# Kernel optimization log

Hardware: AMD Instinct MI355X
Metric: run time of the kernel (lower is better)

Reference implementation:

```python
import jax, jax.numpy as jnp
import numpy as np

N_FR, N_FV, N_REL, N_VAL, N_KN = 512, 512, 256, 256, 512
TOPK_FR, TOPK_FV, TOPK_REL, TOPK_VAL = 8, 8, 4, 6
EPS = 1e-8


def setup_inputs() -> dict:
    key = jax.random.key(0)
    k1, k2, k3, k4 = jax.random.split(key, 4)
    B, S, D, DS = 8, 2048, 2048, 64
    N = N_FR + N_FV + N_REL + N_VAL + N_KN  # 2304
    return {
        "x": jax.random.normal(k1, (B, S, D), dtype=jnp.float32),
        "importance": jax.random.uniform(k2, (B, S), dtype=jnp.float32),
        "W": jax.random.normal(k3, (DS, D), dtype=jnp.float32) * (1.0 / np.sqrt(D)),
        "b": jnp.zeros((DS,), dtype=jnp.float32),
        "neuron_emb": jax.random.normal(k4, (N, DS), dtype=jnp.float32) * 0.02,
    }


def _topk_sparsify(w, k):
    # w: [B, n] -> keep top-k values, zero the rest, renormalize to sum 1
    vals, idx = jax.lax.top_k(w, k)
    B = w.shape[0]
    sparse = jnp.zeros_like(w).at[jnp.arange(B)[:, None], idx].set(vals)
    return sparse / (sparse.sum(axis=-1, keepdims=True) + EPS)


def reference(x, importance, W, b, neuron_emb):
    # Projection (nn.Linear): [B,S,d_space]; dropout is identity in eval mode
    h = jnp.einsum('bsd,kd->bsk', x, W) + b
    # Normalized neuron embeddings (F.normalize along dim=-1)
    emb = neuron_emb / jnp.linalg.norm(neuron_emb, axis=-1, keepdims=True)
    # All routing logits in one shot: [B, S, total_neurons]
    all_logits = jnp.einsum('bsk,nk->bsn', h, emb)

    fr_end = N_FR
    fv_end = N_FR + N_FV
    rel_end = fv_end + N_REL
    val_end = rel_end + N_VAL

    fr_pref = jax.nn.softmax(all_logits[..., :fr_end], axis=-1)
    fv_pref = jax.nn.softmax(all_logits[..., fr_end:fv_end], axis=-1)
    rel_pref = jax.nn.softmax(all_logits[..., fv_end:rel_end], axis=-1)  # shared by Q and K
    val_pref = jax.nn.softmax(all_logits[..., rel_end:val_end], axis=-1)

    def dense(pref):
        return jnp.einsum('bs,bsn->bn', importance, pref)

    fr_w = _topk_sparsify(dense(fr_pref), TOPK_FR)
    fv_w = _topk_sparsify(dense(fv_pref), TOPK_FV)
    rel_d = dense(rel_pref)
    rq_w = _topk_sparsify(rel_d, TOPK_REL)
    rk_w = rq_w  # relational_Q and relational_K slices are identical
    val_w = _topk_sparsify(dense(val_pref), TOPK_VAL)

    # Concatenate the five per-batch routing weight vectors: [B, 512+512+256+256+256]
    return jnp.concatenate([fr_w, fv_w, rq_w, rk_w, val_w], axis=-1)
```

## Files before the change

### kernel.cpp

```cpp
#include <hip/hip_runtime.h>
#include <hip/hip_bf16.h>

#define B_    8
#define S_    2048
#define D_    2048
#define DS_   64
#define NUSED 1536
#define TOK   16384

typedef __attribute__((ext_vector_type(8))) short bf16x8;
typedef __attribute__((ext_vector_type(4))) float f32x4;

static constexpr int WS_ETF  = 0;
static constexpr int WS_HT   = 98304;
static constexpr int WS_PART = 2195456;
static constexpr int WS_PART2= 3768320;
static constexpr int WS_WF   = 3866624;

typedef __attribute__((address_space(1))) const void g_void;
typedef __attribute__((address_space(3))) void l_void;

__device__ inline short bf_hi(float f, float& rhi) {
    __hip_bfloat16 h = __float2bfloat16(f);
    rhi = __bfloat162float(h);
    return __builtin_bit_cast(short, h);
}
__device__ inline short bf_of(float f) {
    __hip_bfloat16 h = __float2bfloat16(f);
    return __builtin_bit_cast(short, h);
}
__device__ inline int sliceOfTile(int tile) {
    return tile < 32 ? 0 : tile < 64 ? 1 : tile < 80 ? 2 : 3;
}

__launch_bounds__(256)
__global__ void k_pre(const float* __restrict__ emb, const float* __restrict__ W,
                      short* __restrict__ etfrag, short* __restrict__ wfrag) {
    __shared__ float red[2][16][8];
    __shared__ float rn[2][16];
    const int tid = threadIdx.x;
    if (blockIdx.x < 48) {
        const int tl = tid >> 7, tid2 = tid & 127;
        const int kh = tid2 >> 6, lane = tid2 & 63;
        const int tile = blockIdx.x * 2 + tl;
        const int nl = lane & 15;
        const int n = tile * 16 + nl;
        const int kb = kh * 32 + (lane >> 4) * 8;
        const float* ep = emb + n * DS_ + kb;
        float4 a = *reinterpret_cast<const float4*>(ep);
        float4 b = *reinterpret_cast<const float4*>(ep + 4);
        float f[8] = {a.x, a.y, a.z, a.w, b.x, b.y, b.z, b.w};
        float ss = 0.f;
#pragma unroll
        for (int j = 0; j < 8; ++j) ss += f[j] * f[j];
        red[tl][nl][kh * 4 + (lane >> 4)] = ss;
        __syncthreads();
        if (tid2 < 16) {
            float s = 0.f;
#pragma unroll
            for (int j = 0; j < 8; ++j) s += red[tl][tid2][j];
            rn[tl][tid2] = 1.0f / sqrtf(s);
        }
        __syncthreads();
        const float r0 = rn[tl][nl];
        bf16x8 hi, lo;
#pragma unroll
        for (int j = 0; j < 8; ++j) {
            float v = f[j] * r0, r;
            hi[j] = bf_hi(v, r);
            lo[j] = bf_of(v - r);
        }
        short* dst = etfrag + (size_t)((tile * 2 + kh) * 64 + lane) * 16;
        *reinterpret_cast<bf16x8*>(dst)     = hi;
        *reinterpret_cast<bf16x8*>(dst + 8) = lo;
    } else {
        const int kstep = blockIdx.x - 48;
        const int msub = tid >> 6, lane = tid & 63;
        const int m = msub * 16 + (lane & 15);
        const float* wp = W + m * D_ + kstep * 32 + (lane >> 4) * 8;
        float4 a = *reinterpret_cast<const float4*>(wp);
        float4 b = *reinterpret_cast<const float4*>(wp + 4);
        float f[8] = {a.x, a.y, a.z, a.w, b.x, b.y, b.z, b.w};
        bf16x8 hi, lo;
#pragma unroll
        for (int j = 0; j < 8; ++j) {
            float r;
            hi[j] = bf_hi(f[j], r);
            lo[j] = bf_of(f[j] - r);
        }
        short* base = wfrag + (size_t)(kstep * 4 + msub) * 1024;
        *reinterpret_cast<bf16x8*>(base + lane * 8)       = hi;
        *reinterpret_cast<bf16x8*>(base + 512 + lane * 8) = lo;
    }
}

#define MFMA16(A, Bv, C) __builtin_amdgcn_mfma_f32_16x16x32_bf16(A, Bv, C, 0, 0, 0)

__launch_bounds__(256, 2)
__global__ void k_gemm1(const float* __restrict__ x, const short* __restrict__ wfrag,
                        float* __restrict__ htp) {
    __shared__ short wlds[2][4][4096];

    const int tid   = threadIdx.x;
    const int split = blockIdx.x & 1;
    const int tb    = (blockIdx.x >> 1) * 64;
    const int wave  = tid >> 6, lane = tid & 63;
    const int tok   = tb + wave * 16 + (lane & 15);

    const float* xp   = x + (size_t)tok * D_ + split * 1024 + (lane >> 4) * 8;
    const short* wsrc = wfrag + (size_t)(split * 32) * 4096;

    f32x4 acc0 = {0.f, 0.f, 0.f, 0.f};
    f32x4 acc1 = acc0, acc2 = acc0, acc3 = acc0;

#define STAGE4(gg, buf)                                                                      \
    {                                                                                        \
        _Pragma("unroll")                                                                    \
        for (int s = 0; s < 4; ++s) {                                                        \
            const short* s0 = wsrc + (size_t)(4 * (gg) + s) * 4096;                          \
            __builtin_amdgcn_global_load_lds((g_void*)(s0 + tid * 8),                        \
                                             (l_void*)(&wlds[buf][s][tid * 8]), 16, 0, 0);   \
            __builtin_amdgcn_global_load_lds((g_void*)(s0 + 2048 + tid * 8),                 \
                                             (l_void*)(&wlds[buf][s][2048 + tid * 8]), 16, 0, 0); \
        }                                                                                    \
    }

    STAGE4(0, 0);
    float4 xc[4], xn[4];
#pragma unroll
    for (int i = 0; i < 4; ++i)
        xc[i] = *reinterpret_cast<const float4*>(xp + (i >> 1) * 32 + (i & 1) * 4);

    for (int g = 0; g < 8; ++g) {
        __syncthreads();
        const int buf = g & 1;
        if (g < 7) STAGE4(g + 1, buf ^ 1);

#pragma unroll
        for (int half = 0; half < 2; ++half) {
            const int hh = g * 2 + half;
            if (hh < 15) {
                const float* nxp = xp + (size_t)(hh + 1) * 64;
#pragma unroll
                for (int i = 0; i < 4; ++i)
                    xn[i] = *reinterpret_cast<const float4*>(nxp + (i >> 1) * 32 + (i & 1) * 4);
            }
#pragma unroll
            for (int kk2 = 0; kk2 < 2; ++kk2) {
                const int kk = half * 2 + kk2;
                const float4 va = xc[kk2 * 2], vb = xc[kk2 * 2 + 1];
                float xf[8] = {va.x, va.y, va.z, va.w, vb.x, vb.y, vb.z, vb.w};
                bf16x8 bh, bl;
#pragma unroll
                for (int j = 0; j < 8; ++j) {
                    float r;
                    bh[j] = bf_hi(xf[j], r);
                    bl[j] = bf_of(xf[j] - r);
                }
                const short* wl = &wlds[buf][kk][0];
                bf16x8 ah0 = *reinterpret_cast<const bf16x8*>(wl +    0 + lane * 8);
                bf16x8 al0 = *reinterpret_cast<const bf16x8*>(wl +  512 + lane * 8);
                bf16x8 ah1 = *reinterpret_cast<const bf16x8*>(wl + 1024 + lane * 8);
                bf16x8 al1 = *reinterpret_cast<const bf16x8*>(wl + 1536 + lane * 8);
                bf16x8 ah2 = *reinterpret_cast<const bf16x8*>(wl + 2048 + lane * 8);
                bf16x8 al2 = *reinterpret_cast<const bf16x8*>(wl + 2560 + lane * 8);
                bf16x8 ah3 = *reinterpret_cast<const bf16x8*>(wl + 3072 + lane * 8);
                bf16x8 al3 = *reinterpret_cast<const bf16x8*>(wl + 3584 + lane * 8);

                acc0 = MFMA16(ah0, bh, acc0);
                acc1 = MFMA16(ah1, bh, acc1);
                acc2 = MFMA16(ah2, bh, acc2);
                acc3 = MFMA16(ah3, bh, acc3);
                acc0 = MFMA16(al0, bh, acc0);
                acc1 = MFMA16(al1, bh, acc1);
                acc2 = MFMA16(al2, bh, acc2);
                acc3 = MFMA16(al3, bh, acc3);
                acc0 = MFMA16(ah0, bl, acc0);
                acc1 = MFMA16(ah1, bl, acc1);
                acc2 = MFMA16(ah2, bl, acc2);
                acc3 = MFMA16(ah3, bl, acc3);
            }
            if (hh < 15) {
#pragma unroll
                for (int i = 0; i < 4; ++i) xc[i] = xn[i];
            }
        }
    }

    const int row0 = split * 64 + (lane >> 4) * 4;
    const int col  = tb + wave * 16 + (lane & 15);
#pragma unroll
    for (int r = 0; r < 4; ++r) {
        htp[(size_t)(row0 +  0 + r) * TOK + col] = acc0[r];
        htp[(size_t)(row0 + 16 + r) * TOK + col] = acc1[r];
        htp[(size_t)(row0 + 32 + r) * TOK + col] = acc2[r];
        htp[(size_t)(row0 + 48 + r) * TOK + col] = acc3[r];
    }
}

__launch_bounds__(512)
__global__ void k_route2(const float* __restrict__ htp, const float* __restrict__ bias,
                         const short* __restrict__ etfrag, const float* __restrict__ imp,
                         float* __restrict__ part) {
    __shared__ float h_lds[64][32];
    __shared__ float zw[2][8][2][16];
    __shared__ float coef[2][4][16];
    __shared__ float impb[32];

    const int tid = threadIdx.x;
    const int w = tid >> 6, lane = tid & 63;
    const int tt2 = blockIdx.x;
    const int tk = lane & 15, g = lane >> 4;

    {
        const int k = tid >> 3, c8 = tid & 7;
        const float4* hp4 = reinterpret_cast<const float4*>(htp);
        const int col = tt2 * 8 + c8;
        float4 a = hp4[(size_t)k * 4096 + col];
        float4 b = hp4[(size_t)(k + 64) * 4096 + col];
        float bk = bias[k];
        float4 s;
        s.x = a.x + b.x + bk;
        s.y = a.y + b.y + bk;
        s.z = a.z + b.z + bk;
        s.w = a.w + b.w + bk;
        *reinterpret_cast<float4*>(&h_lds[k][c8 * 4]) = s;
    }
    if (tid < 32) impb[tid] = imp[tt2 * 32 + tid];
    __syncthreads();

    bf16x8 bh0A, bl0A, bh1A, bl1A, bh0B, bl0B, bh1B, bl1B;
#pragma unroll
    for (int j = 0; j < 8; ++j) {
        float r, v;
        v = h_lds[g * 8 + j][tk];           bh0A[j] = bf_hi(v, r); bl0A[j] = bf_of(v - r);
        v = h_lds[32 + g * 8 + j][tk];      bh1A[j] = bf_hi(v, r); bl1A[j] = bf_of(v - r);
        v = h_lds[g * 8 + j][16 + tk];      bh0B[j] = bf_hi(v, r); bl0B[j] = bf_of(v - r);
        v = h_lds[32 + g * 8 + j][16 + tk]; bh1B[j] = bf_hi(v, r); bl1B[j] = bf_of(v - r);
    }

    const int t0 = w * 12;
    const int sA = sliceOfTile(t0);
    const int sB = sliceOfTile(t0 + 11);
    float zA0 = 0.f, zA1 = 0.f, zB0 = 0.f, zB1 = 0.f;
    float pA[12][4], pB[12][4];

    const short* ep = etfrag + (size_t)t0 * 2048 + lane * 16;
#pragma unroll
    for (int ti = 0; ti < 12; ++ti) {
        const short* cp = ep + (size_t)ti * 2048;
        bf16x8 ah0 = *reinterpret_cast<const bf16x8*>(cp);
        bf16x8 al0 = *reinterpret_cast<const bf16x8*>(cp + 8);
        bf16x8 ah1 = *reinterpret_cast<const bf16x8*>(cp + 1024);
        bf16x8 al1 = *reinterpret_cast<const bf16x8*>(cp + 1032);
        f32x4 a0 = {0.f, 0.f, 0.f, 0.f};
        f32x4 a1 = a0, b0 = a0, b1 = a0;
        a0 = MFMA16(ah0, bh0A, a0);  b0 = MFMA16(ah0, bh0B, b0);
        a1 = MFMA16(ah1, bh1A, a1);  b1 = MFMA16(ah1, bh1B, b1);
        a0 = MFMA16(al0, bh0A, a0);  b0 = MFMA16(al0, bh0B, b0);
        a1 = MFMA16(al1, bh1A, a1);  b1 = MFMA16(al1, bh1B, b1);
        a0 = MFMA16(ah0, bl0A, a0);  b0 = MFMA16(ah0, bl0B, b0);
        a1 = MFMA16(ah1, bl1A, a1);  b1 = MFMA16(ah1, bl1B, b1);

        const float pa0 = __expf(a0[0] + a1[0]);
        const float pa1 = __expf(a0[1] + a1[1]);
        const float pa2 = __expf(a0[2] + a1[2]);
        const float pa3 = __expf(a0[3] + a1[3]);
        pA[ti][0] = pa0; pA[ti][1] = pa1; pA[ti][2] = pa2; pA[ti][3] = pa3;
        const float zsA = (pa0 + pa1) + (pa2 + pa3);
        const float pb0 = __expf(b0[0] + b1[0]);
        const float pb1 = __expf(b0[1] + b1[1]);
        const float pb2 = __expf(b0[2] + b1[2]);
        const float pb3 = __expf(b0[3] + b1[3]);
        pB[ti][0] = pb0; pB[ti][1] = pb1; pB[ti][2] = pb2; pB[ti][3] = pb3;
        const float zsB = (pb0 + pb1) + (pb2 + pb3);
        if (sliceOfTile(t0 + ti) == sA) { zA0 += zsA; zB0 += zsB; }
        else                            { zA1 += zsA; zB1 += zsB; }
    }

    zA0 += __shfl_xor(zA0, 16); zA0 += __shfl_xor(zA0, 32);
    zA1 += __shfl_xor(zA1, 16); zA1 += __shfl_xor(zA1, 32);
    zB0 += __shfl_xor(zB0, 16); zB0 += __shfl_xor(zB0, 32);
    zB1 += __shfl_xor(zB1, 16); zB1 += __shfl_xor(zB1, 32);
    if (lane < 16) {
        zw[0][w][0][lane] = zA0; zw[0][w][1][lane] = zA1;
        zw[1][w][0][lane] = zB0; zw[1][w][1][lane] = zB1;
    }
    __syncthreads();

    if (tid < 128) {
        const int tl = tid >> 6, s = (tid >> 4) & 3, k2 = tid & 15;
        float z = 0.f;
#pragma unroll
        for (int w2 = 0; w2 < 8; ++w2) {
            const int a = sliceOfTile(w2 * 12);
            const int b = sliceOfTile(w2 * 12 + 11);
            if (a == s) z += zw[tl][w2][0][k2];
            if (b == s && b != a) z += zw[tl][w2][1][k2];
        }
        coef[tl][s][k2] = impb[tl * 16 + k2] / z;
    }
    __syncthreads();

    const float cAA = coef[0][sA][tk], cAB = coef[0][sB][tk];
    const float cBA = coef[1][sA][tk], cBB = coef[1][sB][tk];
    float* poutA = part + (size_t)(tt2 * 2) * NUSED;
    float* poutB = poutA + NUSED;
#pragma unroll
    for (int ti = 0; ti < 12; ++ti) {
        const bool inA = (sliceOfTile(t0 + ti) == sA);
        {
            const float c = inA ? cAA : cAB;
            float v0 = pA[ti][0] * c, v1 = pA[ti][1] * c, v2 = pA[ti][2] * c, v3 = pA[ti][3] * c;
#pragma unroll
            for (int st = 1; st < 16; st <<= 1) {
                v0 += __shfl_xor(v0, st);
                v1 += __shfl_xor(v1, st);
                v2 += __shfl_xor(v2, st);
                v3 += __shfl_xor(v3, st);
            }
            if (tk == 0)
                *reinterpret_cast<float4*>(&poutA[(t0 + ti) * 16 + g * 4]) =
                    make_float4(v0, v1, v2, v3);
        }
        {
            const float c = inA ? cBA : cBB;
            float v0 = pB[ti][0] * c, v1 = pB[ti][1] * c, v2 = pB[ti][2] * c, v3 = pB[ti][3] * c;
#pragma unroll
            for (int st = 1; st < 16; st <<= 1) {
                v0 += __shfl_xor(v0, st);
                v1 += __shfl_xor(v1, st);
                v2 += __shfl_xor(v2, st);
                v3 += __shfl_xor(v3, st);
            }
            if (tk == 0)
                *reinterpret_cast<float4*>(&poutB[(t0 + ti) * 16 + g * 4]) =
                    make_float4(v0, v1, v2, v3);
        }
    }
}

__launch_bounds__(256)
__global__ void kA(const float* __restrict__ part, float* __restrict__ part2) {
    const int tid = threadIdx.x;
    const int b = blockIdx.x >> 3, g = blockIdx.x & 7;
    const int base = (b * 128 + g * 16) * NUSED;
#pragma unroll
    for (int i = 0; i < 6; ++i) {
        int n = tid + 256 * i;
        float s = 0.f;
#pragma unroll
        for (int r = 0; r < 16; ++r) s += part[base + r * NUSED + n];
        part2[(b * 8 + g) * NUSED + n] = s;
    }
}

__launch_bounds__(256)
__global__ void kB(const float* __restrict__ part2, float* __restrict__ out) {
    __shared__ float dens[NUSED];
    __shared__ float s_v[4][8];
    __shared__ int   s_n[4][8];
    const int tid = threadIdx.x;
    const int b = blockIdx.x;

#pragma unroll
    for (int i = 0; i < 6; ++i) {
        int n = tid + 256 * i;
        float s = 0.f;
#pragma unroll
        for (int g = 0; g < 8; ++g) s += part2[(b * 8 + g) * NUSED + n];
        dens[n] = s;
    }
    for (int i = tid; i < 1792; i += 256) out[b * 1792 + i] = 0.f;
    __syncthreads();

    const int w = tid >> 6, lane = tid & 63;
    const int soffs[4] = {0, 512, 1024, 1280};
    const int ssz[4]   = {512, 512, 256, 256};
    const int kks[4]   = {8, 8, 4, 6};
    const int ooffs[4] = {0, 512, 1024, 1536};
    const int Sn = ssz[w], soff = soffs[w], kk = kks[w];
    const int nslots = Sn >> 6;

    float v[8];
#pragma unroll
    for (int i = 0; i < 8; ++i)
        v[i] = (i < nslots) ? dens[soff + lane + 64 * i] : -1e30f;

    unsigned rm = 0;
    float ssum = 0.f;
    for (int it = 0; it < kk; ++it) {
        float bv = -1e30f;
        int bn = 0x7fffffff;
#pragma unroll
        for (int i = 0; i < 8; ++i) {
            bool valid = (i < nslots) && !((rm >> i) & 1u);
            if (valid && v[i] > bv) { bv = v[i]; bn = lane + 64 * i; }
        }
#pragma unroll
        for (int off = 32; off; off >>= 1) {
            float ov = __shfl_xor(bv, off);
            int   on = __shfl_xor(bn, off);
            if (ov > bv || (ov == bv && on < bn)) { bv = ov; bn = on; }
        }
        ssum += bv;
        if ((bn & 63) == lane) rm |= 1u << (bn >> 6);
        if (lane == 0) { s_v[w][it] = bv; s_n[w][it] = bn; }
    }
    const float inv = 1.f / (ssum + 1e-8f);
    if (lane < kk) {
        int n = s_n[w][lane];
        float val = s_v[w][lane] * inv;
        out[b * 1792 + ooffs[w] + n] = val;
        if (w == 2) out[b * 1792 + 1280 + n] = val;
    }
}

extern "C" void kernel_launch(void* const* d_in, const int* in_sizes, int n_in,
                              void* d_out, int out_size, void* d_ws, size_t ws_size,
                              hipStream_t stream) {
    const float* x    = (const float*)d_in[0];
    const float* imp  = (const float*)d_in[1];
    const float* W    = (const float*)d_in[2];
    const float* bias = (const float*)d_in[3];
    const float* emb  = (const float*)d_in[4];
    float* out = (float*)d_out;
    float* ws  = (float*)d_ws;

    short* etfrag = (short*)(ws + WS_ETF);
    float* htp    = ws + WS_HT;
    float* part   = ws + WS_PART;
    float* part2  = ws + WS_PART2;
    short* wfrag  = (short*)(ws + WS_WF);

    k_pre<<<112, 256, 0, stream>>>(emb, W, etfrag, wfrag);
    k_gemm1<<<512, 256, 0, stream>>>(x, wfrag, htp);
    k_route2<<<512, 512, 0, stream>>>(htp, bias, etfrag, imp, part);
    kA<<<64, 256, 0, stream>>>(part, part2);
    kB<<<8, 256, 0, stream>>>(part2, out);
}
```

Before: 79.37 us.

## Halve gemm1 LDS staging, widen route2 blocks, fuse final reductions into one kernel

The projection GEMM now stages two k-steps of weight fragments per pipeline step instead of four, halving LDS use and running 16 loop iterations. The routing kernel uses 1024-thread blocks with each wave handling half as many neuron tiles. The two-level partial-sum reduction and top-k kernels are merged into a single kernel with one block per batch that sums all 128 partial rows. This removes one launch and an intermediate buffer, but concentrates the reduction on only 8 blocks.

```diff
diff --git a/kernel.cpp b/kernel.cpp
--- a/kernel.cpp
+++ b/kernel.cpp
@@ -14,8 +14,7 @@
 static constexpr int WS_ETF  = 0;
 static constexpr int WS_HT   = 98304;
 static constexpr int WS_PART = 2195456;
-static constexpr int WS_PART2= 3768320;
-static constexpr int WS_WF   = 3866624;
+static constexpr int WS_WF   = 3768320;
 
 typedef __attribute__((address_space(1))) const void g_void;
 typedef __attribute__((address_space(3))) void l_void;
@@ -99,7 +98,7 @@
 __launch_bounds__(256, 2)
 __global__ void k_gemm1(const float* __restrict__ x, const short* __restrict__ wfrag,
                         float* __restrict__ htp) {
-    __shared__ short wlds[2][4][4096];
+    __shared__ short wlds[2][2][4096];
 
     const int tid   = threadIdx.x;
     const int split = blockIdx.x & 1;
@@ -113,78 +112,74 @@
     f32x4 acc0 = {0.f, 0.f, 0.f, 0.f};
     f32x4 acc1 = acc0, acc2 = acc0, acc3 = acc0;
 
-#define STAGE4(gg, buf)                                                                      \
+#define STAGE(g, buf)                                                                        \
     {                                                                                        \
-        _Pragma("unroll")                                                                    \
-        for (int s = 0; s < 4; ++s) {                                                        \
-            const short* s0 = wsrc + (size_t)(4 * (gg) + s) * 4096;                          \
-            __builtin_amdgcn_global_load_lds((g_void*)(s0 + tid * 8),                        \
-                                             (l_void*)(&wlds[buf][s][tid * 8]), 16, 0, 0);   \
-            __builtin_amdgcn_global_load_lds((g_void*)(s0 + 2048 + tid * 8),                 \
-                                             (l_void*)(&wlds[buf][s][2048 + tid * 8]), 16, 0, 0); \
-        }                                                                                    \
-    }
-
-    STAGE4(0, 0);
-    float4 xc[4], xn[4];
-#pragma unroll
-    for (int i = 0; i < 4; ++i)
-        xc[i] = *reinterpret_cast<const float4*>(xp + (i >> 1) * 32 + (i & 1) * 4);
-
-    for (int g = 0; g < 8; ++g) {
+        const short* s0 = wsrc + (size_t)(2 * (g)) * 4096;                                   \
+        __builtin_amdgcn_global_load_lds((g_void*)(s0 + tid * 8),                            \
+                                         (l_void*)(&wlds[buf][0][tid * 8]), 16, 0, 0);       \
+        __builtin_amdgcn_global_load_lds((g_void*)(s0 + 2048 + tid * 8),                     \
+                                         (l_void*)(&wlds[buf][0][2048 + tid * 8]), 16, 0, 0);\
+        __builtin_amdgcn_global_load_lds((g_void*)(s0 + 4096 + tid * 8),                     \
+                                         (l_void*)(&wlds[buf][1][tid * 8]), 16, 0, 0);       \
+        __builtin_amdgcn_global_load_lds((g_void*)(s0 + 6144 + tid * 8),                     \
+                                         (l_void*)(&wlds[buf][1][2048 + tid * 8]), 16, 0, 0);\
+    }
+
+    STAGE(0, 0);
+    float4 xc0 = *reinterpret_cast<const float4*>(xp);
+    float4 xc1 = *reinterpret_cast<const float4*>(xp + 4);
+    float4 xc2 = *reinterpret_cast<const float4*>(xp + 32);
+    float4 xc3 = *reinterpret_cast<const float4*>(xp + 36);
+
+#pragma unroll 2
+    for (int g = 0; g < 16; ++g) {
         __syncthreads();
         const int buf = g & 1;
-        if (g < 7) STAGE4(g + 1, buf ^ 1);
-
-#pragma unroll
-        for (int half = 0; half < 2; ++half) {
-            const int hh = g * 2 + half;
-            if (hh < 15) {
-                const float* nxp = xp + (size_t)(hh + 1) * 64;
-#pragma unroll
-                for (int i = 0; i < 4; ++i)
-                    xn[i] = *reinterpret_cast<const float4*>(nxp + (i >> 1) * 32 + (i & 1) * 4);
+        float4 xn0, xn1, xn2, xn3;
+        if (g < 15) {
+            STAGE(g + 1, buf ^ 1);
+            const float* nxp = xp + (size_t)(g + 1) * 64;
+            xn0 = *reinterpret_cast<const float4*>(nxp);
+            xn1 = *reinterpret_cast<const float4*>(nxp + 4);
+            xn2 = *reinterpret_cast<const float4*>(nxp + 32);
+            xn3 = *reinterpret_cast<const float4*>(nxp + 36);
+        }
+#pragma unroll
+        for (int kk = 0; kk < 2; ++kk) {
+            const float4 va = kk ? xc2 : xc0;
+            const float4 vb = kk ? xc3 : xc1;
+            float xf[8] = {va.x, va.y, va.z, va.w, vb.x, vb.y, vb.z, vb.w};
+            bf16x8 bh, bl;
+#pragma unroll
+            for (int j = 0; j < 8; ++j) {
+                float r;
+                bh[j] = bf_hi(xf[j], r);
+                bl[j] = bf_of(xf[j] - r);
             }
-#pragma unroll
-            for (int kk2 = 0; kk2 < 2; ++kk2) {
-                const int kk = half * 2 + kk2;
-                const float4 va = xc[kk2 * 2], vb = xc[kk2 * 2 + 1];
-                float xf[8] = {va.x, va.y, va.z, va.w, vb.x, vb.y, vb.z, vb.w};
-                bf16x8 bh, bl;
-#pragma unroll
-                for (int j = 0; j < 8; ++j) {
-                    float r;
-                    bh[j] = bf_hi(xf[j], r);
-                    bl[j] = bf_of(xf[j] - r);
-                }
-                const short* wl = &wlds[buf][kk][0];
-                bf16x8 ah0 = *reinterpret_cast<const bf16x8*>(wl +    0 + lane * 8);
-                bf16x8 al0 = *reinterpret_cast<const bf16x8*>(wl +  512 + lane * 8);
-                bf16x8 ah1 = *reinterpret_cast<const bf16x8*>(wl + 1024 + lane * 8);
-                bf16x8 al1 = *reinterpret_cast<const bf16x8*>(wl + 1536 + lane * 8);
-                bf16x8 ah2 = *reinterpret_cast<const bf16x8*>(wl + 2048 + lane * 8);
-                bf16x8 al2 = *reinterpret_cast<const bf16x8*>(wl + 2560 + lane * 8);
-                bf16x8 ah3 = *reinterpret_cast<const bf16x8*>(wl + 3072 + lane * 8);
-                bf16x8 al3 = *reinterpret_cast<const bf16x8*>(wl + 3584 + lane * 8);
-
-                acc0 = MFMA16(ah0, bh, acc0);
-                acc1 = MFMA16(ah1, bh, acc1);
-                acc2 = MFMA16(ah2, bh, acc2);
-                acc3 = MFMA16(ah3, bh, acc3);
-                acc0 = MFMA16(al0, bh, acc0);
-                acc1 = MFMA16(al1, bh, acc1);
-                acc2 = MFMA16(al2, bh, acc2);
-                acc3 = MFMA16(al3, bh, acc3);
-                acc0 = MFMA16(ah0, bl, acc0);
-                acc1 = MFMA16(ah1, bl, acc1);
-                acc2 = MFMA16(ah2, bl, acc2);
-                acc3 = MFMA16(ah3, bl, acc3);
-            }
-            if (hh < 15) {
-#pragma unroll
-                for (int i = 0; i < 4; ++i) xc[i] = xn[i];
-            }
-        }
+            const short* wl = &wlds[buf][kk][0];
+            bf16x8 ah0 = *reinterpret_cast<const bf16x8*>(wl +    0 + lane * 8);
+            bf16x8 al0 = *reinterpret_cast<const bf16x8*>(wl +  512 + lane * 8);
+            bf16x8 ah1 = *reinterpret_cast<const bf16x8*>(wl + 1024 + lane * 8);
+            bf16x8 al1 = *reinterpret_cast<const bf16x8*>(wl + 1536 + lane * 8);
+            bf16x8 ah2 = *reinterpret_cast<const bf16x8*>(wl + 2048 + lane * 8);
+            bf16x8 al2 = *reinterpret_cast<const bf16x8*>(wl + 2560 + lane * 8);
+            bf16x8 ah3 = *reinterpret_cast<const bf16x8*>(wl + 3072 + lane * 8);
+            bf16x8 al3 = *reinterpret_cast<const bf16x8*>(wl + 3584 + lane * 8);
+
+            acc0 = MFMA16(ah0, bh, acc0);
+            acc1 = MFMA16(ah1, bh, acc1);
+            acc2 = MFMA16(ah2, bh, acc2);
+            acc3 = MFMA16(ah3, bh, acc3);
+            acc0 = MFMA16(al0, bh, acc0);
+            acc1 = MFMA16(al1, bh, acc1);
+            acc2 = MFMA16(al2, bh, acc2);
+            acc3 = MFMA16(al3, bh, acc3);
+            acc0 = MFMA16(ah0, bl, acc0);
+            acc1 = MFMA16(ah1, bl, acc1);
+            acc2 = MFMA16(ah2, bl, acc2);
+            acc3 = MFMA16(ah3, bl, acc3);
+        }
+        if (g < 15) { xc0 = xn0; xc1 = xn1; xc2 = xn2; xc3 = xn3; }
     }
 
     const int row0 = split * 64 + (lane >> 4) * 4;
@@ -198,12 +193,12 @@
     }
 }
 
-__launch_bounds__(512)
+__launch_bounds__(1024)
 __global__ void k_route2(const float* __restrict__ htp, const float* __restrict__ bias,
                          const short* __restrict__ etfrag, const float* __restrict__ imp,
                          float* __restrict__ part) {
     __shared__ float h_lds[64][32];
-    __shared__ float zw[2][8][2][16];
+    __shared__ float zw[2][16][2][16];
     __shared__ float coef[2][4][16];
     __shared__ float impb[32];
 
@@ -212,7 +207,7 @@
     const int tt2 = blockIdx.x;
     const int tk = lane & 15, g = lane >> 4;
 
-    {
+    if (tid < 512) {
         const int k = tid >> 3, c8 = tid & 7;
         const float4* hp4 = reinterpret_cast<const float4*>(htp);
         const int col = tt2 * 8 + c8;
@@ -239,15 +234,15 @@
         v = h_lds[32 + g * 8 + j][16 + tk]; bh1B[j] = bf_hi(v, r); bl1B[j] = bf_of(v - r);
     }
 
-    const int t0 = w * 12;
+    const int t0 = w * 6;
     const int sA = sliceOfTile(t0);
-    const int sB = sliceOfTile(t0 + 11);
+    const int sB = sliceOfTile(t0 + 5);
     float zA0 = 0.f, zA1 = 0.f, zB0 = 0.f, zB1 = 0.f;
-    float pA[12][4], pB[12][4];
+    float pA[6][4], pB[6][4];
 
     const short* ep = etfrag + (size_t)t0 * 2048 + lane * 16;
 #pragma unroll
-    for (int ti = 0; ti < 12; ++ti) {
+    for (int ti = 0; ti < 6; ++ti) {
         const short* cp = ep + (size_t)ti * 2048;
         bf16x8 ah0 = *reinterpret_cast<const bf16x8*>(cp);
         bf16x8 al0 = *reinterpret_cast<const bf16x8*>(cp + 8);
@@ -292,9 +287,9 @@
         const int tl = tid >> 6, s = (tid >> 4) & 3, k2 = tid & 15;
         float z = 0.f;
 #pragma unroll
-        for (int w2 = 0; w2 < 8; ++w2) {
-            const int a = sliceOfTile(w2 * 12);
-            const int b = sliceOfTile(w2 * 12 + 11);
+        for (int w2 = 0; w2 < 16; ++w2) {
+            const int a = sliceOfTile(w2 * 6);
+            const int b = sliceOfTile(w2 * 6 + 5);
             if (a == s) z += zw[tl][w2][0][k2];
             if (b == s && b != a) z += zw[tl][w2][1][k2];
         }
@@ -307,7 +302,7 @@
     float* poutA = part + (size_t)(tt2 * 2) * NUSED;
     float* poutB = poutA + NUSED;
 #pragma unroll
-    for (int ti = 0; ti < 12; ++ti) {
+    for (int ti = 0; ti < 6; ++ti) {
         const bool inA = (sliceOfTile(t0 + ti) == sA);
         {
             const float c = inA ? cAA : cAB;
@@ -340,79 +335,69 @@
     }
 }
 
-__launch_bounds__(256)
-__global__ void kA(const float* __restrict__ part, float* __restrict__ part2) {
-    const int tid = threadIdx.x;
-    const int b = blockIdx.x >> 3, g = blockIdx.x & 7;
-    const int base = (b * 128 + g * 16) * NUSED;
-#pragma unroll
-    for (int i = 0; i < 6; ++i) {
-        int n = tid + 256 * i;
-        float s = 0.f;
-#pragma unroll
-        for (int r = 0; r < 16; ++r) s += part[base + r * NUSED + n];
-        part2[(b * 8 + g) * NUSED + n] = s;
-    }
-}
-
-__launch_bounds__(256)
-__global__ void kB(const float* __restrict__ part2, float* __restrict__ out) {
+__launch_bounds__(1024)
+__global__ void kAB(const float* __restrict__ part, float* __restrict__ out) {
     __shared__ float dens[NUSED];
     __shared__ float s_v[4][8];
     __shared__ int   s_n[4][8];
     const int tid = threadIdx.x;
     const int b = blockIdx.x;
-
-#pragma unroll
-    for (int i = 0; i < 6; ++i) {
-        int n = tid + 256 * i;
-        float s = 0.f;
-#pragma unroll
-        for (int g = 0; g < 8; ++g) s += part2[(b * 8 + g) * NUSED + n];
-        dens[n] = s;
-    }
-    for (int i = tid; i < 1792; i += 256) out[b * 1792 + i] = 0.f;
+    const float* pb = part + (size_t)(b * 128) * NUSED;
+
+#pragma unroll
+    for (int i = 0; i < 2; ++i) {
+        int n = tid + 1024 * i;
+        if (n < NUSED) {
+            float s = 0.f;
+#pragma unroll 8
+            for (int r = 0; r < 128; ++r) s += pb[(size_t)r * NUSED + n];
+            dens[n] = s;
+        }
+    }
+    for (int i = tid; i < 1792; i += 1024) out[b * 1792 + i] = 0.f;
     __syncthreads();
 
     const int w = tid >> 6, lane = tid & 63;
-    const int soffs[4] = {0, 512, 1024, 1280};
-    const int ssz[4]   = {512, 512, 256, 256};
-    const int kks[4]   = {8, 8, 4, 6};
-    const int ooffs[4] = {0, 512, 1024, 1536};
-    const int Sn = ssz[w], soff = soffs[w], kk = kks[w];
-    const int nslots = Sn >> 6;
-
-    float v[8];
-#pragma unroll
-    for (int i = 0; i < 8; ++i)
-        v[i] = (i < nslots) ? dens[soff + lane + 64 * i] : -1e30f;
-
-    unsigned rm = 0;
-    float ssum = 0.f;
-    for (int it = 0; it < kk; ++it) {
-        float bv = -1e30f;
-        int bn = 0x7fffffff;
-#pragma unroll
-        for (int i = 0; i < 8; ++i) {
-            bool valid = (i < nslots) && !((rm >> i) & 1u);
-            if (valid && v[i] > bv) { bv = v[i]; bn = lane + 64 * i; }
-        }
-#pragma unroll
-        for (int off = 32; off; off >>= 1) {
-            float ov = __shfl_xor(bv, off);
-            int   on = __shfl_xor(bn, off);
-            if (ov > bv || (ov == bv && on < bn)) { bv = ov; bn = on; }
-        }
-        ssum += bv;
-        if ((bn & 63) == lane) rm |= 1u << (bn >> 6);
-        if (lane == 0) { s_v[w][it] = bv; s_n[w][it] = bn; }
-    }
-    const float inv = 1.f / (ssum + 1e-8f);
-    if (lane < kk) {
-        int n = s_n[w][lane];
-        float val = s_v[w][lane] * inv;
-        out[b * 1792 + ooffs[w] + n] = val;
-        if (w == 2) out[b * 1792 + 1280 + n] = val;
+    if (w < 4) {
+        const int soffs[4] = {0, 512, 1024, 1280};
+        const int ssz[4]   = {512, 512, 256, 256};
+        const int kks[4]   = {8, 8, 4, 6};
+        const int ooffs[4] = {0, 512, 1024, 1536};
+        const int Sn = ssz[w], soff = soffs[w], kk = kks[w];
+        const int nslots = Sn >> 6;
+
+        float v[8];
+#pragma unroll
+        for (int i = 0; i < 8; ++i)
+            v[i] = (i < nslots) ? dens[soff + lane + 64 * i] : -1e30f;
+
+        unsigned rm = 0;
+        float ssum = 0.f;
+        for (int it = 0; it < kk; ++it) {
+            float bv = -1e30f;
+            int bn = 0x7fffffff;
+#pragma unroll
+            for (int i = 0; i < 8; ++i) {
+                bool valid = (i < nslots) && !((rm >> i) & 1u);
+                if (valid && v[i] > bv) { bv = v[i]; bn = lane + 64 * i; }
+            }
+#pragma unroll
+            for (int off = 32; off; off >>= 1) {
+                float ov = __shfl_xor(bv, off);
+                int   on = __shfl_xor(bn, off);
+                if (ov > bv || (ov == bv && on < bn)) { bv = ov; bn = on; }
+            }
+            ssum += bv;
+            if ((bn & 63) == lane) rm |= 1u << (bn >> 6);
+            if (lane == 0) { s_v[w][it] = bv; s_n[w][it] = bn; }
+        }
+        const float inv = 1.f / (ssum + 1e-8f);
+        if (lane < kk) {
+            int n = s_n[w][lane];
+            float val = s_v[w][lane] * inv;
+            out[b * 1792 + ooffs[w] + n] = val;
+            if (w == 2) out[b * 1792 + 1280 + n] = val;
+        }
     }
 }
 
@@ -430,12 +415,10 @@
     short* etfrag = (short*)(ws + WS_ETF);
     float* htp    = ws + WS_HT;
     float* part   = ws + WS_PART;
-    float* part2  = ws + WS_PART2;
     short* wfrag  = (short*)(ws + WS_WF);
 
     k_pre<<<112, 256, 0, stream>>>(emb, W, etfrag, wfrag);
     k_gemm1<<<512, 256, 0, stream>>>(x, wfrag, htp);
-    k_route2<<<512, 512, 0, stream>>>(htp, bias, etfrag, imp, part);
-    kA<<<64, 256, 0, stream>>>(part, part2);
-    kB<<<8, 256, 0, stream>>>(part2, out);
-}
+    k_route2<<<512, 1024, 0, stream>>>(htp, bias, etfrag, imp, part);
+    kAB<<<B_, 1024, 0, stream>>>(part, out);
+}
```

Result: slower. 93.03 us (+17.2%).
